# Kernel optimization log

Measured on AMD Instinct MI355X. Metric: run time of the kernel, lower is better.

Reference implementation:

```python
import jax, jax.numpy as jnp
import numpy as np

WIN = 9
WIN_SIZE = float(WIN ** 3)
LBD = 1.0
EPS = 1e-5


def _box_sum(x, win=WIN):
    """Separable sum over a win^3 window with zero padding == conv3d with all-ones kernel."""
    pad = win // 2
    for ax in (2, 3, 4):  # spatial axes of [N, C, H, W, D]
        wd = [1] * 5
        wd[ax] = win
        padc = [(0, 0)] * 5
        padc[ax] = (pad, pad)
        x = jax.lax.reduce_window(x, 0.0, jax.lax.add, tuple(wd), (1, 1, 1, 1, 1), padc)
    return x


def _warp3d(images, flows):
    """Trilinear warp. images [B,G,C,H,W,D], flows [B,G,3,H,W,D] (voxel displacements,
    channels ordered as (H, W, D) axes). Border-clamped sampling."""
    B, G, C, H, W, D = images.shape
    N = B * G
    img = images.reshape(N, C, H, W, D)
    flo = flows.reshape(N, 3, H, W, D)
    ft = flo.dtype
    gh = jnp.arange(H, dtype=ft).reshape(H, 1, 1)
    gw = jnp.arange(W, dtype=ft).reshape(1, W, 1)
    gd = jnp.arange(D, dtype=ft).reshape(1, 1, D)
    ch = jnp.clip(flo[:, 0] + gh, 0.0, H - 1.0)
    cw = jnp.clip(flo[:, 1] + gw, 0.0, W - 1.0)
    cd = jnp.clip(flo[:, 2] + gd, 0.0, D - 1.0)
    h0f = jnp.floor(ch); w0f = jnp.floor(cw); d0f = jnp.floor(cd)
    fh = ch - h0f; fw = cw - w0f; fd = cd - d0f
    h0 = h0f.astype(jnp.int32); w0 = w0f.astype(jnp.int32); d0 = d0f.astype(jnp.int32)
    h1 = jnp.minimum(h0 + 1, H - 1)
    w1 = jnp.minimum(w0 + 1, W - 1)
    d1 = jnp.minimum(d0 + 1, D - 1)
    flat = img.reshape(N, C, H * W * D)

    def gather(hi, wi, di):
        lin = ((hi * W + wi) * D + di).reshape(N, 1, H * W * D)
        return jnp.take_along_axis(flat, lin, axis=2).reshape(N, C, H, W, D)

    out = jnp.zeros_like(img)
    for hi, wh in ((h0, 1.0 - fh), (h1, fh)):
        for wi, ww in ((w0, 1.0 - fw), (w1, fw)):
            for di, wdw in ((d0, 1.0 - fd), (d1, fd)):
                w8 = (wh * ww * wdw)[:, None]  # [N,1,H,W,D]
                out = out + w8 * gather(hi, wi, di)
    return out.reshape(B, G, C, H, W, D)


def setup_inputs() -> dict:
    key = jax.random.key(0)
    k1, k2 = jax.random.split(key)
    images = jax.random.normal(k1, (1, 4, 1, 128, 128, 128), dtype=jnp.float32)
    warps = jax.random.normal(k2, (1, 4, 3, 128, 128, 128), dtype=jnp.float32)
    return {"images": images, "warps": warps}


def reference(images, warps):
    B, G, C, H, W, D = images.shape
    warped = _warp3d(images, warps).reshape(B * G, C, H, W, D)
    # groupwise template = mean over the B*G warped volumes, broadcast back
    template = jnp.broadcast_to(jnp.mean(warped, axis=0, keepdims=True), warped.shape)
    Ii, Ji = template, warped
    # 5 stat channels: I, J, I^2, J^2, IJ; groups=5 box-filter conv == per-channel box sum
    stats = jnp.concatenate([Ii, Ji, Ii * Ii, Ji * Ji, Ii * Ji], axis=1)
    sums = _box_sum(stats)
    I_sum, J_sum, I2_sum, J2_sum, IJ_sum = jnp.split(sums, 5, axis=1)
    cross = IJ_sum - J_sum / WIN_SIZE * I_sum
    I_var = I2_sum - I_sum / WIN_SIZE * I_sum
    J_var = J2_sum - J_sum / WIN_SIZE * J_sum
    cc = cross * cross / (I_var * J_var + EPS)
    lncc = -jnp.mean(cc)
    # Grad3d('l2') on warps [B,G,3,H,W,D]: dx over H (axis 3), dy over W (axis 4), dz over D (axis 5)
    dx = jnp.square(warps[:, :, :, 1:] - warps[:, :, :, :-1])
    dy = jnp.square(warps[:, :, :, :, 1:] - warps[:, :, :, :, :-1])
    dz = jnp.square(warps[..., 1:] - warps[..., :-1])
    g2 = (jnp.mean(dx) + jnp.mean(dy) + jnp.mean(dz)) / 3.0
    return lncc + LBD * g2
```

## Files before the change

### kernel.cpp

```cpp
#include <hip/hip_runtime.h>
#include <hip/hip_bf16.h>


#define NVOX (128*128*128)
#define NGRP 4
#define NCH 14

typedef float f32x4 __attribute__((ext_vector_type(4)));
typedef float f32x2 __attribute__((ext_vector_type(2)));

__global__ __launch_bounds__(256) void k_pack2(const float* __restrict__ img,
                                               f32x2* __restrict__ P2)
{
    int idx = blockIdx.x * 256 + threadIdx.x;
    int v = idx & (NVOX - 1);
    int g = idx >> 21;
    int d = v & 127;
    const float* im = img + (size_t)g * NVOX;
    float a = im[v];
    float b = (d < 127) ? im[v + 1] : a;
    f32x2 pv; pv.x = a; pv.y = b;
    __builtin_nontemporal_store(pv, &P2[idx]);
}

__global__ __launch_bounds__(256) void k_warp_stats_d(
    const f32x2* __restrict__ P2, const float* __restrict__ flo,
    float* __restrict__ S, double* __restrict__ pg2)
{
    __shared__ float jt[NGRP][256];
    int t = threadIdx.x;
    int b = ((blockIdx.x & 7) << 10) | (blockIdx.x >> 3);
    int v = b * 256 + t;
    int d = v & 127;
    int w = (v >> 7) & 127;
    int h = v >> 14;
    float g2s = 0.f;

#pragma unroll
    for (int g = 0; g < NGRP; ++g) {
        const float* f = flo + (size_t)g * 3 * NVOX;
        float fx = f[v], fy = f[NVOX + v], fz = f[2 * NVOX + v];
        if (h < 127) {
            float a = f[v + 16384] - fx;
            float bb = f[NVOX + v + 16384] - fy;
            float c = f[2 * NVOX + v + 16384] - fz;
            g2s += a * a + bb * bb + c * c;
        }
        if (w < 127) {
            float a = f[v + 128] - fx;
            float bb = f[NVOX + v + 128] - fy;
            float c = f[2 * NVOX + v + 128] - fz;
            g2s += a * a + bb * bb + c * c;
        }
        if (d < 127) {
            float a = f[v + 1] - fx;
            float bb = f[NVOX + v + 1] - fy;
            float c = f[2 * NVOX + v + 1] - fz;
            g2s += a * a + bb * bb + c * c;
        }
        float ch = fminf(fmaxf(fx + (float)h, 0.f), 127.f);
        float cw = fminf(fmaxf(fy + (float)w, 0.f), 127.f);
        float cd = fminf(fmaxf(fz + (float)d, 0.f), 127.f);
        float h0f = floorf(ch), w0f = floorf(cw), d0f = floorf(cd);
        int h0 = (int)h0f, w0 = (int)w0f, d0 = (int)d0f;
        float fh = ch - h0f, fw = cw - w0f, fd = cd - d0f;
        int h1 = min(h0 + 1, 127), w1 = min(w0 + 1, 127);
        const f32x2* P = P2 + (size_t)g * NVOX;
        f32x2 q00 = P[h0 * 16384 + w0 * 128 + d0];
        f32x2 q01 = P[h0 * 16384 + w1 * 128 + d0];
        f32x2 q10 = P[h1 * 16384 + w0 * 128 + d0];
        f32x2 q11 = P[h1 * 16384 + w1 * 128 + d0];
        float c00 = q00.x + fd * (q00.y - q00.x);
        float c01 = q01.x + fd * (q01.y - q01.x);
        float c10 = q10.x + fd * (q10.y - q10.x);
        float c11 = q11.x + fd * (q11.y - q11.x);
        float c0 = c00 + fw * (c01 - c00);
        float c1 = c10 + fw * (c11 - c10);
        jt[g][t] = c0 + fh * (c1 - c0);
    }
    __syncthreads();

    float s[NCH];
#pragma unroll
    for (int c = 0; c < NCH; ++c) s[c] = 0.f;
    int lbase = t & 128;
#pragma unroll
    for (int k = -4; k <= 4; ++k) {
        int q = d + k;
        if ((unsigned)q < 128u) {
            int tq = lbase + q;
            float j0 = jt[0][tq], j1 = jt[1][tq], j2 = jt[2][tq], j3 = jt[3][tq];
            float tm = 0.25f * (j0 + j1 + j2 + j3);
            s[0] += tm;       s[1] += tm * tm;
            s[2] += j0;  s[3] += j0 * j0;  s[4]  += tm * j0;
            s[5] += j1;  s[6] += j1 * j1;  s[7]  += tm * j1;
            s[8] += j2;  s[9] += j2 * j2;  s[10] += tm * j2;
            s[11] += j3; s[12] += j3 * j3; s[13] += tm * j3;
        }
    }
#pragma unroll
    for (int c = 0; c < NCH; ++c)
        __builtin_nontemporal_store(s[c], &S[(size_t)c * NVOX + v]);

    double val = (double)g2s;
    for (int off = 32; off; off >>= 1) val += __shfl_down(val, off, 64);
    __shared__ double wsum[4];
    int lane = t & 63, wid = t >> 6;
    if (lane == 0) wsum[wid] = val;
    __syncthreads();
    if (t == 0) pg2[b] = wsum[0] + wsum[1] + wsum[2] + wsum[3];
}

__global__ __launch_bounds__(256) void k_sum_w(float* __restrict__ S)
{
    __shared__ float tile[128 * 68];
    int t = threadIdx.x;
    int bid = blockIdx.x;
    int half = bid & 1;
    int chh = bid >> 1;
    size_t base = (size_t)chh * 16384 + half * 64;
#pragma unroll
    for (int it = 0; it < 8; ++it) {
        int idx4 = it * 256 + t;
        int w = idx4 >> 4, dq = idx4 & 15;
        f32x4 vv = __builtin_nontemporal_load(
            (const f32x4*)(S + base + (size_t)w * 128 + dq * 4));
        *(f32x4*)(tile + w * 68 + dq * 4) = vv;
    }
    __syncthreads();
    int dq = t & 15;
    int wq = t >> 4;
    int w0 = wq * 8;
    f32x4 s = {0.f, 0.f, 0.f, 0.f};
#pragma unroll
    for (int k = -4; k <= 4; ++k) {
        int q = w0 + k;
        if ((unsigned)q < 128u)
            s += *(const f32x4*)(tile + q * 68 + dq * 4);
    }
    __builtin_nontemporal_store(s, (f32x4*)(S + base + (size_t)w0 * 128 + dq * 4));
#pragma unroll
    for (int wi = 1; wi < 8; ++wi) {
        int w = w0 + wi;
        int qa = w + 4;
        if (qa < 128)
            s += *(const f32x4*)(tile + qa * 68 + dq * 4);
        int qr = w - 5;
        if (qr >= 0)
            s -= *(const f32x4*)(tile + qr * 68 + dq * 4);
        __builtin_nontemporal_store(s, (f32x4*)(S + base + (size_t)w * 128 + dq * 4));
    }
}

__device__ __forceinline__ float cc4(f32x4 I, f32x4 I2, f32x4 J, f32x4 J2, f32x4 IJ)
{
    const float inv = 1.0f / 729.0f;
    f32x4 cr = IJ - J * I * inv;
    f32x4 iv = I2 - I * I * inv;
    f32x4 jv = J2 - J * J * inv;
    f32x4 cc = cr * cr / (iv * jv + 1e-5f);
    return cc.x + cc.y + cc.z + cc.w;
}

#define LOADH(c, a0, a1)                                                       \
    do {                                                                       \
        const float* cp = S + (size_t)(c) * NVOX + cbase;                      \
        _Pragma("unroll")                                                      \
        for (int it = 0; it < 3; ++it) {                                       \
            int idx = it * 256 + t;                                            \
            if (idx < 640) {                           \
                int row = idx >> 4, dqu = idx & 15;                            \
                int rr = r0 + row;                                             \
                f32x4 vv = {0.f, 0.f, 0.f, 0.f};                               \
                if ((unsigned)rr < 128u)                                       \
                    vv = __builtin_nontemporal_load(                           \
                        (const f32x4*)(cp + (size_t)rr * 16384 + dqu * 4));    \
                int la = row * 65 + dqu * 4;                                   \
                tile[la] = vv.x; tile[la + 1] = vv.y;                          \
                tile[la + 2] = vv.z; tile[la + 3] = vv.w;                      \
            }                                                                  \
        }                                                                      \
        __syncthreads();                                                       \
        {                                                                      \
            int hl = hg * 2;                                                   \
            f32x4 sum = {0.f, 0.f, 0.f, 0.f};                                  \
            _Pragma("unroll")                                                  \
            for (int k = 0; k < 9; ++k) {                                      \
                const float* tp = tile + (hl + k) * 65 + dq * 4;               \
                sum.x += tp[0]; sum.y += tp[1]; sum.z += tp[2]; sum.w += tp[3];\
            }                                                                  \
            a0 = sum;                                                          \
            const float* ta = tile + (hl + 9) * 65 + dq * 4;                   \
            const float* tr = tile + hl * 65 + dq * 4;                         \
            sum.x += ta[0] - tr[0]; sum.y += ta[1] - tr[1];                    \
            sum.z += ta[2] - tr[2]; sum.w += ta[3] - tr[3];                    \
            a1 = sum;                                                          \
        }                                                                      \
        __syncthreads();                                                       \
    } while (0)

__global__ __launch_bounds__(256) void k_sum_h_cc(const float* __restrict__ S,
                                                  double* __restrict__ pcc)
{
    __shared__ float tile[40 * 65];
    int t = threadIdx.x;
    int bid = blockIdx.x;
    int dh = bid & 1;
    int hq = (bid >> 1) & 3;
    int w = bid >> 3;
    int r0 = hq * 32 - 4;
    size_t cbase = (size_t)w * 128 + dh * 64;
    int dq = t & 15;
    int hg = t >> 4;

    f32x4 Ia0, Ia1, I2a0, I2a1, Ja0, Ja1, J2a0, J2a1, IJa0, IJa1;
    float lsum = 0.f;

    LOADH(0, Ia0, Ia1);
    LOADH(1, I2a0, I2a1);
    for (int g = 0; g < NGRP; ++g) {
        LOADH(2 + 3 * g, Ja0, Ja1);
        LOADH(3 + 3 * g, J2a0, J2a1);
        LOADH(4 + 3 * g, IJa0, IJa1);
        lsum += cc4(Ia0, I2a0, Ja0, J2a0, IJa0);
        lsum += cc4(Ia1, I2a1, Ja1, J2a1, IJa1);
    }

    double val = (double)lsum;
    for (int off = 32; off; off >>= 1) val += __shfl_down(val, off, 64);
    __shared__ double wsum[4];
    int lane = t & 63, wid = t >> 6;
    if (lane == 0) wsum[wid] = val;
    __syncthreads();
    if (t == 0) pcc[bid] = wsum[0] + wsum[1] + wsum[2] + wsum[3];
}

__global__ __launch_bounds__(256) void k_finalize(const double* __restrict__ pg2,
                                                  const double* __restrict__ pcc,
                                                  float* __restrict__ out)
{
    double s_cc = 0.0, s_g2 = 0.0;
    for (int i = threadIdx.x; i < 1024; i += 256) s_cc += pcc[i];
    for (int i = threadIdx.x; i < 8192; i += 256) s_g2 += pg2[i];
    for (int off = 32; off; off >>= 1) {
        s_cc += __shfl_down(s_cc, off, 64);
        s_g2 += __shfl_down(s_g2, off, 64);
    }
    __shared__ double a[4], b[4];
    int lane = threadIdx.x & 63, wid = threadIdx.x >> 6;
    if (lane == 0) { a[wid] = s_cc; b[wid] = s_g2; }
    __syncthreads();
    if (threadIdx.x == 0) {
        double cc_sum = a[0] + a[1] + a[2] + a[3];
        double g2_sum = b[0] + b[1] + b[2] + b[3];
        double lncc = -cc_sum / (4.0 * (double)NVOX);
        double g2 = g2_sum / (3.0 * 12.0 * 127.0 * 128.0 * 128.0);
        out[0] = (float)(lncc + g2);
    }
}

extern "C" void kernel_launch(void* const* d_in, const int* in_sizes, int n_in,
                              void* d_out, int out_size, void* d_ws, size_t ws_size,
                              hipStream_t stream)
{
    const float* img = (const float*)d_in[0];
    const float* flo = (const float*)d_in[1];
    float* out = (float*)d_out;

    const size_t S_BYTES  = (size_t)NCH * NVOX * 4;
    const size_t P2_BYTES = (size_t)NGRP * NVOX * 8;
    float* S = (float*)d_ws;
    f32x2* P2 = (f32x2*)((char*)d_ws + S_BYTES);
    double* pg2 = (double*)((char*)d_ws + S_BYTES + P2_BYTES);
    double* pcc = pg2 + 8192;

    k_pack2<<<(NGRP * NVOX) / 256, 256, 0, stream>>>(img, P2);
    k_warp_stats_d<<<NVOX / 256, 256, 0, stream>>>(P2, flo, S, pg2);
    k_sum_w<<<NCH * 128 * 2, 256, 0, stream>>>(S);
    k_sum_h_cc<<<1024, 256, 0, stream>>>(S, pcc);
    k_finalize<<<1, 256, 0, stream>>>(pg2, pcc, out);
}
```

Before: 408.9 us.

## Drop packed image pre-pass and batch trilinear gathers directly from image

```diff
diff --git a/kernel.cpp b/kernel.cpp
--- a/kernel.cpp
+++ b/kernel.cpp
@@ -7,24 +7,9 @@
 #define NCH 14
 
 typedef float f32x4 __attribute__((ext_vector_type(4)));
-typedef float f32x2 __attribute__((ext_vector_type(2)));
-
-__global__ __launch_bounds__(256) void k_pack2(const float* __restrict__ img,
-                                               f32x2* __restrict__ P2)
-{
-    int idx = blockIdx.x * 256 + threadIdx.x;
-    int v = idx & (NVOX - 1);
-    int g = idx >> 21;
-    int d = v & 127;
-    const float* im = img + (size_t)g * NVOX;
-    float a = im[v];
-    float b = (d < 127) ? im[v + 1] : a;
-    f32x2 pv; pv.x = a; pv.y = b;
-    __builtin_nontemporal_store(pv, &P2[idx]);
-}
-
-__global__ __launch_bounds__(256) void k_warp_stats_d(
-    const f32x2* __restrict__ P2, const float* __restrict__ flo,
+
+__global__ __launch_bounds__(256, 2) void k_warp_stats_d(
+    const float* __restrict__ img, const float* __restrict__ flo,
     float* __restrict__ S, double* __restrict__ pg2)
 {
     __shared__ float jt[NGRP][256];
@@ -34,49 +19,79 @@
     int d = v & 127;
     int w = (v >> 7) & 127;
     int h = v >> 14;
-    float g2s = 0.f;
-
+
+    float fx[NGRP], fy[NGRP], fz[NGRP];
 #pragma unroll
     for (int g = 0; g < NGRP; ++g) {
         const float* f = flo + (size_t)g * 3 * NVOX;
-        float fx = f[v], fy = f[NVOX + v], fz = f[2 * NVOX + v];
-        if (h < 127) {
-            float a = f[v + 16384] - fx;
-            float bb = f[NVOX + v + 16384] - fy;
-            float c = f[2 * NVOX + v + 16384] - fz;
-            g2s += a * a + bb * bb + c * c;
-        }
-        if (w < 127) {
-            float a = f[v + 128] - fx;
-            float bb = f[NVOX + v + 128] - fy;
-            float c = f[2 * NVOX + v + 128] - fz;
-            g2s += a * a + bb * bb + c * c;
-        }
-        if (d < 127) {
-            float a = f[v + 1] - fx;
-            float bb = f[NVOX + v + 1] - fy;
-            float c = f[2 * NVOX + v + 1] - fz;
-            g2s += a * a + bb * bb + c * c;
-        }
-        float ch = fminf(fmaxf(fx + (float)h, 0.f), 127.f);
-        float cw = fminf(fmaxf(fy + (float)w, 0.f), 127.f);
-        float cd = fminf(fmaxf(fz + (float)d, 0.f), 127.f);
+        fx[g] = f[v];
+        fy[g] = f[NVOX + v];
+        fz[g] = f[2 * NVOX + v];
+    }
+
+    float fh[NGRP], fw[NGRP], fd[NGRP];
+    int o[NGRP][4];
+    int d1o[NGRP];
+#pragma unroll
+    for (int g = 0; g < NGRP; ++g) {
+        float ch = fminf(fmaxf(fx[g] + (float)h, 0.f), 127.f);
+        float cw = fminf(fmaxf(fy[g] + (float)w, 0.f), 127.f);
+        float cd = fminf(fmaxf(fz[g] + (float)d, 0.f), 127.f);
         float h0f = floorf(ch), w0f = floorf(cw), d0f = floorf(cd);
         int h0 = (int)h0f, w0 = (int)w0f, d0 = (int)d0f;
-        float fh = ch - h0f, fw = cw - w0f, fd = cd - d0f;
+        fh[g] = ch - h0f; fw[g] = cw - w0f; fd[g] = cd - d0f;
         int h1 = min(h0 + 1, 127), w1 = min(w0 + 1, 127);
-        const f32x2* P = P2 + (size_t)g * NVOX;
-        f32x2 q00 = P[h0 * 16384 + w0 * 128 + d0];
-        f32x2 q01 = P[h0 * 16384 + w1 * 128 + d0];
-        f32x2 q10 = P[h1 * 16384 + w0 * 128 + d0];
-        f32x2 q11 = P[h1 * 16384 + w1 * 128 + d0];
-        float c00 = q00.x + fd * (q00.y - q00.x);
-        float c01 = q01.x + fd * (q01.y - q01.x);
-        float c10 = q10.x + fd * (q10.y - q10.x);
-        float c11 = q11.x + fd * (q11.y - q11.x);
-        float c0 = c00 + fw * (c01 - c00);
-        float c1 = c10 + fw * (c11 - c10);
-        jt[g][t] = c0 + fh * (c1 - c0);
+        d1o[g] = (d0 < 127) ? 1 : 0;
+        o[g][0] = (h0 * 128 + w0) * 128 + d0;
+        o[g][1] = (h0 * 128 + w1) * 128 + d0;
+        o[g][2] = (h1 * 128 + w0) * 128 + d0;
+        o[g][3] = (h1 * 128 + w1) * 128 + d0;
+    }
+
+    float gv[NGRP][8];
+#pragma unroll
+    for (int g = 0; g < NGRP; ++g) {
+        const float* im = img + (size_t)g * NVOX;
+        gv[g][0] = im[o[g][0]]; gv[g][1] = im[o[g][0] + d1o[g]];
+        gv[g][2] = im[o[g][1]]; gv[g][3] = im[o[g][1] + d1o[g]];
+        gv[g][4] = im[o[g][2]]; gv[g][5] = im[o[g][2] + d1o[g]];
+        gv[g][6] = im[o[g][3]]; gv[g][7] = im[o[g][3] + d1o[g]];
+    }
+    __builtin_amdgcn_sched_barrier(0);
+
+    float g2s = 0.f;
+#pragma unroll
+    for (int g = 0; g < NGRP; ++g) {
+        const float* f = flo + (size_t)g * 3 * NVOX;
+        if (h < 127) {
+            float a = f[v + 16384] - fx[g];
+            float bb = f[NVOX + v + 16384] - fy[g];
+            float c = f[2 * NVOX + v + 16384] - fz[g];
+            g2s += a * a + bb * bb + c * c;
+        }
+        if (w < 127) {
+            float a = f[v + 128] - fx[g];
+            float bb = f[NVOX + v + 128] - fy[g];
+            float c = f[2 * NVOX + v + 128] - fz[g];
+            g2s += a * a + bb * bb + c * c;
+        }
+        if (d < 127) {
+            float a = f[v + 1] - fx[g];
+            float bb = f[NVOX + v + 1] - fy[g];
+            float c = f[2 * NVOX + v + 1] - fz[g];
+            g2s += a * a + bb * bb + c * c;
+        }
+    }
+
+#pragma unroll
+    for (int g = 0; g < NGRP; ++g) {
+        float c00 = gv[g][0] + fd[g] * (gv[g][1] - gv[g][0]);
+        float c01 = gv[g][2] + fd[g] * (gv[g][3] - gv[g][2]);
+        float c10 = gv[g][4] + fd[g] * (gv[g][5] - gv[g][4]);
+        float c11 = gv[g][6] + fd[g] * (gv[g][7] - gv[g][6]);
+        float c0 = c00 + fw[g] * (c01 - c00);
+        float c1 = c10 + fw[g] * (c11 - c10);
+        jt[g][t] = c0 + fh[g] * (c1 - c0);
     }
     __syncthreads();
 
@@ -267,15 +282,12 @@
     const float* flo = (const float*)d_in[1];
     float* out = (float*)d_out;
 
-    const size_t S_BYTES  = (size_t)NCH * NVOX * 4;
-    const size_t P2_BYTES = (size_t)NGRP * NVOX * 8;
+    const size_t S_BYTES = (size_t)NCH * NVOX * 4;
     float* S = (float*)d_ws;
-    f32x2* P2 = (f32x2*)((char*)d_ws + S_BYTES);
-    double* pg2 = (double*)((char*)d_ws + S_BYTES + P2_BYTES);
+    double* pg2 = (double*)((char*)d_ws + S_BYTES);
     double* pcc = pg2 + 8192;
 
-    k_pack2<<<(NGRP * NVOX) / 256, 256, 0, stream>>>(img, P2);
-    k_warp_stats_d<<<NVOX / 256, 256, 0, stream>>>(P2, flo, S, pg2);
+    k_warp_stats_d<<<NVOX / 256, 256, 0, stream>>>(img, flo, S, pg2);
     k_sum_w<<<NCH * 128 * 2, 256, 0, stream>>>(S);
     k_sum_h_cc<<<1024, 256, 0, stream>>>(S, pcc);
     k_finalize<<<1, 256, 0, stream>>>(pg2, pcc, out);
```

Result: faster. 353.2 us (-13.6%).
